# Performance work log

Hardware: AMD Instinct MI355X
Metric: run time of the kernel (lower is better)

Reference implementation:

```python
import jax, jax.numpy as jnp
import numpy as np

T = 3          # num_node_type
B = 8          # batch
N = 512        # max_doc_len
F_IN = 256     # in_features
F_OUT = 128    # out_features
NE = 10        # num_edge_type (embedding has NE+1 rows, row 0 = padding)
ALPHA = 0.2    # leaky relu slope
NEG = -9e15    # masked-score fill, same constant as torch source


def setup_inputs() -> dict:
    key = jax.random.key(0)
    ks = jax.random.split(key, 7)
    node_rep = jax.random.normal(ks[0], (B, N, F_IN), jnp.float32)
    node_type_mask_rep = jax.random.uniform(ks[1], (T, B, N, 1), jnp.float32)
    adj = jax.random.randint(ks[2], (B, N, N), 0, NE + 1, jnp.int32)
    W = jax.random.normal(ks[3], (T, F_IN, F_OUT), jnp.float32) * 0.05
    b = jnp.zeros((T, F_OUT), jnp.float32)
    # attention vector a in R^{2F} split into halves (GAT trick): a([h_i, x2_ij]) = h_i.a1 + x2_ij.a2 + a_b
    a1 = jax.random.normal(ks[4], (F_OUT,), jnp.float32) * 0.05
    a2 = jax.random.normal(ks[5], (F_OUT,), jnp.float32) * 0.05
    a_b = jnp.zeros((), jnp.float32)
    emb = jax.random.normal(ks[6], (NE + 1, F_OUT), jnp.float32) * 0.05
    emb = emb.at[0].set(0.0)  # padding_idx=0
    return {"node_rep": node_rep, "node_type_mask_rep": node_type_mask_rep,
            "adj": adj, "W": W, "b": b, "a1": a1, "a2": a2, "a_b": a_b, "emb": emb}


def reference(node_rep, node_type_mask_rep, adj, W, b, a1, a2, a_b, emb):
    # typed projection: h = sum_t (node_rep @ W_t + b_t) * mask_t   -> (B, N, F_OUT)
    h = jnp.sum((jnp.einsum('bni,tio->tbno', node_rep, W) + b[:, None, None, :])
                * node_type_mask_rep, axis=0)
    # edge-type embeddings: (B, N, N, F_OUT)
    E = emb[adj]
    # x_2[b,i,j] = h[b,j] + E[b,i,j]
    x2 = h[:, None, :, :] + E
    # score[b,i,j] = leakyrelu(a1.h_i + a2.x2_ij + a_b)  (decomposed concat-linear)
    s = (jnp.einsum('bif,f->bi', h, a1)[:, :, None]
         + jnp.einsum('bijf,f->bij', x2, a2) + a_b)
    s = jnp.where(s > 0, s, ALPHA * s)
    s = jnp.where(adj > 0, s, jnp.float32(NEG))
    attn = jax.nn.softmax(s, axis=2)
    # weighted sum over neighbors of x_2 (NOT h), then ELU
    out = jnp.einsum('bij,bijf->bif', attn, x2)
    return jax.nn.elu(out)
```

## Files before the change

kernel.cpp:

```cpp
#include <hip/hip_runtime.h>

constexpr int kB    = 8;
constexpr int kN    = 512;
constexpr int kFIN  = 256;
constexpr int kFOUT = 128;
constexpr int kNE   = 10;
constexpr int kBN   = kB * kN;
constexpr float kALPHA = 0.2f;
constexpr float kNEG   = -9e15f;

typedef __attribute__((ext_vector_type(8))) short bhalf8;
typedef __attribute__((ext_vector_type(4))) float f32x4;

__device__ __forceinline__ unsigned short bf16_trunc(float x) {
    union { float f; unsigned u; } c; c.f = x;
    return (unsigned short)(c.u >> 16);
}
__device__ __forceinline__ float bf16_tof(unsigned short h) {
    union { unsigned u; float f; } c; c.u = ((unsigned)h) << 16;
    return c.f;
}

__global__ __launch_bounds__(256) void prep_kernel(
    const float* __restrict__ node_rep,
    const float* __restrict__ W,
    unsigned short* __restrict__ Xh,
    unsigned short* __restrict__ Xl,
    unsigned short* __restrict__ Whp,
    unsigned short* __restrict__ Wlp)
{
    const int tid = threadIdx.x;
    if (blockIdx.x < 1024) {
        const int gid  = blockIdx.x * 256 + tid;
        const size_t base = (size_t)gid * 4;
        const float4 v = *(const float4*)&node_rep[base];
        ushort4 hi, lo;
        float t;
        hi.x = bf16_trunc(v.x); t = v.x - bf16_tof(hi.x); lo.x = bf16_trunc(t);
        hi.y = bf16_trunc(v.y); t = v.y - bf16_tof(hi.y); lo.y = bf16_trunc(t);
        hi.z = bf16_trunc(v.z); t = v.z - bf16_tof(hi.z); lo.z = bf16_trunc(t);
        hi.w = bf16_trunc(v.w); t = v.w - bf16_tof(hi.w); lo.w = bf16_trunc(t);
        *(ushort4*)&Xh[base] = hi;
        *(ushort4*)&Xl[base] = lo;
    } else {
        const int g    = (blockIdx.x - 1024) * 256 + tid;
        const int lane = g & 63;
        const int nt   = (g >> 6) & 7;
        const int ks   = (g >> 9) & 7;
        const int tt   = g >> 12;
        const int col  = nt * 16 + (lane & 15);
        const int kb   = ks * 32 + ((lane >> 4) * 8);
        unsigned short hbuf[8], lbuf[8];
        #pragma unroll
        for (int j = 0; j < 8; ++j) {
            const float w = W[((size_t)tt * kFIN + kb + j) * kFOUT + col];
            hbuf[j] = bf16_trunc(w);
            lbuf[j] = bf16_trunc(w - bf16_tof(hbuf[j]));
        }
        const size_t dst = ((size_t)((tt * 8 + ks) * 8 + nt)) * 512 + lane * 8;
        #pragma unroll
        for (int j = 0; j < 8; ++j) { Whp[dst + j] = hbuf[j]; Wlp[dst + j] = lbuf[j]; }
    }
}

__global__ __launch_bounds__(256) void proj_mfma_kernel(
    const unsigned short* __restrict__ Xh,
    const unsigned short* __restrict__ Xl,
    const unsigned short* __restrict__ Whp,
    const unsigned short* __restrict__ Wlp,
    float* __restrict__ y)
{
    const int tid   = threadIdx.x;
    const int t     = blockIdx.x % 3;
    const int rb    = blockIdx.x / 3;
    const int wave  = tid >> 6;
    const int lane  = tid & 63;
    const int wrow  = wave & 1;
    const int whalf = wave >> 1;

    const int rowA = rb * 32 + wrow * 16 + (lane & 15);
    const unsigned short* xhp = Xh + (size_t)rowA * kFIN + ((lane >> 4) * 8);
    const unsigned short* xlp = Xl + (size_t)rowA * kFIN + ((lane >> 4) * 8);

    f32x4 acc[4] = {{0,0,0,0},{0,0,0,0},{0,0,0,0},{0,0,0,0}};

    #pragma unroll
    for (int ks = 0; ks < 8; ++ks) {
        const bhalf8 Ah = *(const bhalf8*)(xhp + ks * 32);
        const bhalf8 Al = *(const bhalf8*)(xlp + ks * 32);
        const size_t bw = ((size_t)((t * 8 + ks) * 8 + whalf * 4)) * 512 + lane * 8;
        #pragma unroll
        for (int n = 0; n < 4; ++n) {
            const bhalf8 Bh = *(const bhalf8*)(Whp + bw + n * 512);
            const bhalf8 Bl = *(const bhalf8*)(Wlp + bw + n * 512);
            acc[n] = __builtin_amdgcn_mfma_f32_16x16x32_bf16(Ah, Bh, acc[n], 0, 0, 0);
            acc[n] = __builtin_amdgcn_mfma_f32_16x16x32_bf16(Ah, Bl, acc[n], 0, 0, 0);
            acc[n] = __builtin_amdgcn_mfma_f32_16x16x32_bf16(Al, Bh, acc[n], 0, 0, 0);
        }
    }

    const int rbase = rb * 32 + wrow * 16 + ((lane >> 4) * 4);
    const int cbase = whalf * 64 + (lane & 15);
    #pragma unroll
    for (int n = 0; n < 4; ++n)
        #pragma unroll
        for (int j = 0; j < 4; ++j)
            y[((size_t)t * kBN + rbase + j) * kFOUT + cbase + n * 16] = acc[n][j];
}

__global__ __launch_bounds__(256) void reduce_kernel(
    const float* __restrict__ y,
    const float* __restrict__ mask,
    const float* __restrict__ bias,
    const float* __restrict__ a1,
    const float* __restrict__ a2,
    const float* __restrict__ a_b,
    const float* __restrict__ emb,
    float* __restrict__ h,
    float* __restrict__ s1,
    float* __restrict__ s2,
    float* __restrict__ emb_a2)
{
    __shared__ float hls[8][kFOUT];

    const int tid  = threadIdx.x;
    const int row0 = blockIdx.x * 8;
    const int o    = tid & 127;
    const int rh   = tid >> 7;

    #pragma unroll
    for (int rr = 0; rr < 4; ++rr) {
        const int r   = rh * 4 + rr;
        const int row = row0 + r;
        const float hv =
              mask[0 * kBN + row] * (y[((size_t)0 * kBN + row) * kFOUT + o] + bias[0 * kFOUT + o])
            + mask[1 * kBN + row] * (y[((size_t)1 * kBN + row) * kFOUT + o] + bias[1 * kFOUT + o])
            + mask[2 * kBN + row] * (y[((size_t)2 * kBN + row) * kFOUT + o] + bias[2 * kFOUT + o]);
        h[(size_t)row * kFOUT + o] = hv;
        hls[r][o] = hv;
    }
    __syncthreads();

    {
        const int wv = tid >> 6, lane = tid & 63;
        #pragma unroll
        for (int rr = 0; rr < 2; ++rr) {
            const int r = wv * 2 + rr;
            const float v0 = hls[r][lane];
            const float v1 = hls[r][64 + lane];
            float p1 = v0 * a1[lane] + v1 * a1[64 + lane];
            float p2 = v0 * a2[lane] + v1 * a2[64 + lane];
            #pragma unroll
            for (int off = 32; off; off >>= 1) {
                p1 += __shfl_down(p1, off);
                p2 += __shfl_down(p2, off);
            }
            if (lane == 0) {
                s1[row0 + r] = p1 + a_b[0];
                s2[row0 + r] = p2;
            }
        }
    }

    if (blockIdx.x == 0 && tid < 176) {
        const int e = tid >> 4, l = tid & 15;
        float p = 0.f;
        #pragma unroll
        for (int k8 = 0; k8 < 8; ++k8)
            p += emb[e * kFOUT + l + k8 * 16] * a2[l + k8 * 16];
        #pragma unroll
        for (int off = 8; off; off >>= 1) p += __shfl_xor(p, off);
        if (l == 0) emb_a2[e] = p;
    }
}

__global__ __launch_bounds__(512) void attn_kernel(
    const int*   __restrict__ adj,
    const float* __restrict__ emb,
    const float* __restrict__ h,
    const float* __restrict__ s1,
    const float* __restrict__ s2,
    const float* __restrict__ emb_a2g,
    float* __restrict__ out)
{
    __shared__ float sc[8][kN + 4];
    __shared__ int   adjs[8][kN];
    __shared__ float scT[kN][8];
    __shared__ float wsum[8][16];
    __shared__ float ea2[16];

    const int tid = threadIdx.x;
    const int b   = blockIdx.x >> 6;
    const int i0  = (blockIdx.x & 63) * 8;

    if (tid < 16) ea2[tid] = emb_a2g[tid];
    __syncthreads();

    const int*   adjb = adj + ((size_t)(b * kN + i0)) * kN;
    const float* s2b  = s2 + b * kN;
    #pragma unroll
    for (int it = 0; it < 2; ++it) {
        const int idx = tid + it * 512;
        const int r = idx >> 7, jq = idx & 127;
        const int4   av  = *(const int4*)&adjb[(size_t)r * kN + jq * 4];
        const float4 s2v = *(const float4*)&s2b[jq * 4];
        const float  sr  = s1[b * kN + i0 + r];
        float4 sv; float s;
        s = sr + s2v.x + ea2[av.x]; s = s > 0.f ? s : kALPHA * s; sv.x = av.x > 0 ? s : kNEG;
        s = sr + s2v.y + ea2[av.y]; s = s > 0.f ? s : kALPHA * s; sv.y = av.y > 0 ? s : kNEG;
        s = sr + s2v.z + ea2[av.z]; s = s > 0.f ? s : kALPHA * s; sv.z = av.z > 0 ? s : kNEG;
        s = sr + s2v.w + ea2[av.w]; s = s > 0.f ? s : kALPHA * s; sv.w = av.w > 0 ? s : kNEG;
        *(float4*)&sc[r][jq * 4] = sv;
        *(int4*)&adjs[r][jq * 4] = av;
    }
    __syncthreads();

    {
        const int r = tid >> 6, lane = tid & 63;
        float v[8]; int av[8];
        #pragma unroll
        for (int k = 0; k < 8; ++k) {
            v[k]  = sc[r][lane + k * 64];
            av[k] = adjs[r][lane + k * 64];
        }
        float m = v[0];
        #pragma unroll
        for (int k = 1; k < 8; ++k) m = fmaxf(m, v[k]);
        #pragma unroll
        for (int off = 32; off; off >>= 1) m = fmaxf(m, __shfl_xor(m, off));
        float sum = 0.f;
        #pragma unroll
        for (int k = 0; k < 8; ++k) { v[k] = __expf(v[k] - m); sum += v[k]; }
        #pragma unroll
        for (int off = 32; off; off >>= 1) sum += __shfl_xor(sum, off);
        const float inv = 1.0f / sum;
        #pragma unroll
        for (int k = 0; k < 8; ++k) {
            v[k] *= inv;
            scT[lane + k * 64][r] = v[k];
        }
        #pragma unroll
        for (int e = 1; e <= kNE; ++e) {
            float p = 0.f;
            #pragma unroll
            for (int k = 0; k < 8; ++k) p += (av[k] == e) ? v[k] : 0.f;
            #pragma unroll
            for (int off = 32; off; off >>= 1) p += __shfl_xor(p, off);
            if (lane == 0) wsum[r][e] = p;
        }
    }
    __syncthreads();

    const int f4l = tid & 31;
    const int rg  = (tid >> 5) & 1;
    const int js  = tid >> 6;
    const float* hb  = h + ((size_t)(b * kN + js * 64)) * kFOUT + f4l * 4;
    const float* sct = &scT[js * 64][rg * 4];

    float4 acc0 = {0,0,0,0}, acc1 = {0,0,0,0}, acc2 = {0,0,0,0}, acc3 = {0,0,0,0};
    #pragma unroll 4
    for (int jj = 0; jj < 64; ++jj) {
        const float4 w4 = *(const float4*)&sct[jj * 8];
        const float4 hv = *(const float4*)&hb[(size_t)jj * kFOUT];
        acc0.x = fmaf(w4.x, hv.x, acc0.x); acc0.y = fmaf(w4.x, hv.y, acc0.y);
        acc0.z = fmaf(w4.x, hv.z, acc0.z); acc0.w = fmaf(w4.x, hv.w, acc0.w);
        acc1.x = fmaf(w4.y, hv.x, acc1.x); acc1.y = fmaf(w4.y, hv.y, acc1.y);
        acc1.z = fmaf(w4.y, hv.z, acc1.z); acc1.w = fmaf(w4.y, hv.w, acc1.w);
        acc2.x = fmaf(w4.z, hv.x, acc2.x); acc2.y = fmaf(w4.z, hv.y, acc2.y);
        acc2.z = fmaf(w4.z, hv.z, acc2.z); acc2.w = fmaf(w4.z, hv.w, acc2.w);
        acc3.x = fmaf(w4.w, hv.x, acc3.x); acc3.y = fmaf(w4.w, hv.y, acc3.y);
        acc3.z = fmaf(w4.w, hv.z, acc3.z); acc3.w = fmaf(w4.w, hv.w, acc3.w);
    }
    __syncthreads();

    float* parts_lo = (float*)adjs;
    float* parts_hi = (float*)sc;
    {
        float* pbase = (js < 4) ? parts_lo + js * 1024
                                : parts_hi + (js - 4) * 1024;
        const int rbase = rg * 4;
        *(float4*)&pbase[(rbase + 0) * kFOUT + f4l * 4] = acc0;
        *(float4*)&pbase[(rbase + 1) * kFOUT + f4l * 4] = acc1;
        *(float4*)&pbase[(rbase + 2) * kFOUT + f4l * 4] = acc2;
        *(float4*)&pbase[(rbase + 3) * kFOUT + f4l * 4] = acc3;
    }
    __syncthreads();

    if (tid < 256) {
        const int r  = tid >> 5;
        const int fl = (tid & 31) * 4;
        float4 a = {0,0,0,0};
        #pragma unroll
        for (int p = 0; p < 4; ++p) {
            const float4 v0 = *(const float4*)&parts_lo[p * 1024 + r * kFOUT + fl];
            const float4 v1 = *(const float4*)&parts_hi[p * 1024 + r * kFOUT + fl];
            a.x += v0.x + v1.x; a.y += v0.y + v1.y;
            a.z += v0.z + v1.z; a.w += v0.w + v1.w;
        }
        #pragma unroll
        for (int e = 1; e <= kNE; ++e) {
            const float  wv = wsum[r][e];
            const float4 ev = *(const float4*)&emb[e * kFOUT + fl];
            a.x = fmaf(wv, ev.x, a.x); a.y = fmaf(wv, ev.y, a.y);
            a.z = fmaf(wv, ev.z, a.z); a.w = fmaf(wv, ev.w, a.w);
        }
        a.x = a.x > 0.f ? a.x : expm1f(a.x);
        a.y = a.y > 0.f ? a.y : expm1f(a.y);
        a.z = a.z > 0.f ? a.z : expm1f(a.z);
        a.w = a.w > 0.f ? a.w : expm1f(a.w);
        *(float4*)&out[((size_t)(b * kN + i0 + r)) * kFOUT + fl] = a;
    }
}

extern "C" void kernel_launch(void* const* d_in, const int* in_sizes, int n_in,
                              void* d_out, int out_size, void* d_ws, size_t ws_size,
                              hipStream_t stream) {
    const float* node_rep = (const float*)d_in[0];
    const float* mask     = (const float*)d_in[1];
    const int*   adj      = (const int*)  d_in[2];
    const float* W        = (const float*)d_in[3];
    const float* bias     = (const float*)d_in[4];
    const float* a1       = (const float*)d_in[5];
    const float* a2       = (const float*)d_in[6];
    const float* a_b      = (const float*)d_in[7];
    const float* emb      = (const float*)d_in[8];
    float* out = (float*)d_out;

    float* fws    = (float*)d_ws;
    float* h      = fws;
    float* s1     = h + (size_t)kBN * kFOUT;
    float* s2     = s1 + kBN;
    float* emb_a2 = s2 + kBN;
    float* y      = emb_a2 + 64;
    unsigned short* Xh  = (unsigned short*)(y + (size_t)3 * kBN * kFOUT);
    unsigned short* Xl  = Xh + (size_t)kBN * kFIN;
    unsigned short* Whp = Xl + (size_t)kBN * kFIN;
    unsigned short* Wlp = Whp + 3 * 8 * 8 * 512;

    prep_kernel<<<1072, 256, 0, stream>>>(node_rep, W, Xh, Xl, Whp, Wlp);
    proj_mfma_kernel<<<384, 256, 0, stream>>>(Xh, Xl, Whp, Wlp, y);
    reduce_kernel<<<kBN / 8, 256, 0, stream>>>(
        y, mask, bias, a1, a2, a_b, emb, h, s1, s2, emb_a2);
    attn_kernel<<<kBN / 8, 512, 0, stream>>>(
        adj, emb, h, s1, s2, emb_a2, out);
}
```

Before: 108.7 us.

## Fuse bf16 split, typed projection and score reduction into one kernel

```diff
diff --git a/kernel.cpp b/kernel.cpp
--- a/kernel.cpp
+++ b/kernel.cpp
@@ -22,28 +22,16 @@
 }
 
 __global__ __launch_bounds__(256) void prep_kernel(
-    const float* __restrict__ node_rep,
     const float* __restrict__ W,
-    unsigned short* __restrict__ Xh,
-    unsigned short* __restrict__ Xl,
+    const float* __restrict__ emb,
+    const float* __restrict__ a2,
     unsigned short* __restrict__ Whp,
-    unsigned short* __restrict__ Wlp)
+    unsigned short* __restrict__ Wlp,
+    float* __restrict__ emb_a2)
 {
     const int tid = threadIdx.x;
-    if (blockIdx.x < 1024) {
-        const int gid  = blockIdx.x * 256 + tid;
-        const size_t base = (size_t)gid * 4;
-        const float4 v = *(const float4*)&node_rep[base];
-        ushort4 hi, lo;
-        float t;
-        hi.x = bf16_trunc(v.x); t = v.x - bf16_tof(hi.x); lo.x = bf16_trunc(t);
-        hi.y = bf16_trunc(v.y); t = v.y - bf16_tof(hi.y); lo.y = bf16_trunc(t);
-        hi.z = bf16_trunc(v.z); t = v.z - bf16_tof(hi.z); lo.z = bf16_trunc(t);
-        hi.w = bf16_trunc(v.w); t = v.w - bf16_tof(hi.w); lo.w = bf16_trunc(t);
-        *(ushort4*)&Xh[base] = hi;
-        *(ushort4*)&Xl[base] = lo;
-    } else {
-        const int g    = (blockIdx.x - 1024) * 256 + tid;
+    if (blockIdx.x < 48) {
+        const int g    = blockIdx.x * 256 + tid;
         const int lane = g & 63;
         const int nt   = (g >> 6) & 7;
         const int ks   = (g >> 9) & 7;
@@ -60,117 +48,120 @@
         const size_t dst = ((size_t)((tt * 8 + ks) * 8 + nt)) * 512 + lane * 8;
         #pragma unroll
         for (int j = 0; j < 8; ++j) { Whp[dst + j] = hbuf[j]; Wlp[dst + j] = lbuf[j]; }
-    }
-}
-
-__global__ __launch_bounds__(256) void proj_mfma_kernel(
-    const unsigned short* __restrict__ Xh,
-    const unsigned short* __restrict__ Xl,
+    } else if (tid < 176) {
+        const int e = tid >> 4, l = tid & 15;
+        float p = 0.f;
+        #pragma unroll
+        for (int k8 = 0; k8 < 8; ++k8)
+            p += emb[e * kFOUT + l + k8 * 16] * a2[l + k8 * 16];
+        #pragma unroll
+        for (int off = 8; off; off >>= 1) p += __shfl_xor(p, off);
+        if (l == 0) emb_a2[e] = p;
+    }
+}
+
+__global__ __launch_bounds__(512) void proj_kernel(
+    const float* __restrict__ node_rep,
+    const float* __restrict__ mask,
+    const float* __restrict__ bias,
     const unsigned short* __restrict__ Whp,
     const unsigned short* __restrict__ Wlp,
-    float* __restrict__ y)
-{
-    const int tid   = threadIdx.x;
-    const int t     = blockIdx.x % 3;
-    const int rb    = blockIdx.x / 3;
-    const int wave  = tid >> 6;
-    const int lane  = tid & 63;
-    const int wrow  = wave & 1;
-    const int whalf = wave >> 1;
-
-    const int rowA = rb * 32 + wrow * 16 + (lane & 15);
-    const unsigned short* xhp = Xh + (size_t)rowA * kFIN + ((lane >> 4) * 8);
-    const unsigned short* xlp = Xl + (size_t)rowA * kFIN + ((lane >> 4) * 8);
-
-    f32x4 acc[4] = {{0,0,0,0},{0,0,0,0},{0,0,0,0},{0,0,0,0}};
-
-    #pragma unroll
-    for (int ks = 0; ks < 8; ++ks) {
-        const bhalf8 Ah = *(const bhalf8*)(xhp + ks * 32);
-        const bhalf8 Al = *(const bhalf8*)(xlp + ks * 32);
-        const size_t bw = ((size_t)((t * 8 + ks) * 8 + whalf * 4)) * 512 + lane * 8;
-        #pragma unroll
-        for (int n = 0; n < 4; ++n) {
-            const bhalf8 Bh = *(const bhalf8*)(Whp + bw + n * 512);
-            const bhalf8 Bl = *(const bhalf8*)(Wlp + bw + n * 512);
-            acc[n] = __builtin_amdgcn_mfma_f32_16x16x32_bf16(Ah, Bh, acc[n], 0, 0, 0);
-            acc[n] = __builtin_amdgcn_mfma_f32_16x16x32_bf16(Ah, Bl, acc[n], 0, 0, 0);
-            acc[n] = __builtin_amdgcn_mfma_f32_16x16x32_bf16(Al, Bh, acc[n], 0, 0, 0);
-        }
-    }
-
-    const int rbase = rb * 32 + wrow * 16 + ((lane >> 4) * 4);
-    const int cbase = whalf * 64 + (lane & 15);
-    #pragma unroll
-    for (int n = 0; n < 4; ++n)
-        #pragma unroll
-        for (int j = 0; j < 4; ++j)
-            y[((size_t)t * kBN + rbase + j) * kFOUT + cbase + n * 16] = acc[n][j];
-}
-
-__global__ __launch_bounds__(256) void reduce_kernel(
-    const float* __restrict__ y,
-    const float* __restrict__ mask,
-    const float* __restrict__ bias,
     const float* __restrict__ a1,
     const float* __restrict__ a2,
     const float* __restrict__ a_b,
-    const float* __restrict__ emb,
     float* __restrict__ h,
     float* __restrict__ s1,
-    float* __restrict__ s2,
-    float* __restrict__ emb_a2)
+    float* __restrict__ s2)
 {
-    __shared__ float hls[8][kFOUT];
+    __shared__ short xsh[32][264];
+    __shared__ short xsl[32][264];
 
     const int tid  = threadIdx.x;
-    const int row0 = blockIdx.x * 8;
-    const int o    = tid & 127;
-    const int rh   = tid >> 7;
+    const int row0 = blockIdx.x * 32;
+
+    #pragma unroll
+    for (int it = 0; it < 4; ++it) {
+        const int idx = tid + it * 512;
+        const int r = idx >> 6, q = idx & 63;
+        const float4 v = *(const float4*)&node_rep[(size_t)(row0 + r) * kFIN + q * 4];
+        ushort4 hi, lo;
+        hi.x = bf16_trunc(v.x); lo.x = bf16_trunc(v.x - bf16_tof(hi.x));
+        hi.y = bf16_trunc(v.y); lo.y = bf16_trunc(v.y - bf16_tof(hi.y));
+        hi.z = bf16_trunc(v.z); lo.z = bf16_trunc(v.z - bf16_tof(hi.z));
+        hi.w = bf16_trunc(v.w); lo.w = bf16_trunc(v.w - bf16_tof(hi.w));
+        *(ushort4*)&xsh[r][q * 4] = hi;
+        *(ushort4*)&xsl[r][q * 4] = lo;
+    }
+    __syncthreads();
+
+    const int wave = tid >> 6, lane = tid & 63;
+    const int wrow = wave & 1, wcol = wave >> 1;
+    const int arow = wrow * 16 + (lane & 15);
+    const int koff = (lane >> 4) * 8;
+
+    f32x4 acc[3][2];
+    #pragma unroll
+    for (int t = 0; t < 3; ++t)
+        #pragma unroll
+        for (int nt = 0; nt < 2; ++nt) acc[t][nt] = (f32x4){0,0,0,0};
+
+    #pragma unroll 2
+    for (int ks = 0; ks < 8; ++ks) {
+        const bhalf8 Ah = *(const bhalf8*)&xsh[arow][ks * 32 + koff];
+        const bhalf8 Al = *(const bhalf8*)&xsl[arow][ks * 32 + koff];
+        #pragma unroll
+        for (int t = 0; t < 3; ++t)
+            #pragma unroll
+            for (int nt = 0; nt < 2; ++nt) {
+                const size_t bw =
+                    ((size_t)((t * 8 + ks) * 8 + wcol * 2 + nt)) * 512 + lane * 8;
+                const bhalf8 Bh = *(const bhalf8*)(Whp + bw);
+                const bhalf8 Bl = *(const bhalf8*)(Wlp + bw);
+                acc[t][nt] = __builtin_amdgcn_mfma_f32_16x16x32_bf16(Ah, Bh, acc[t][nt], 0, 0, 0);
+                acc[t][nt] = __builtin_amdgcn_mfma_f32_16x16x32_bf16(Ah, Bl, acc[t][nt], 0, 0, 0);
+                acc[t][nt] = __builtin_amdgcn_mfma_f32_16x16x32_bf16(Al, Bh, acc[t][nt], 0, 0, 0);
+            }
+    }
+    __syncthreads();
+
+    float* hstash = (float*)xsh;
+
+    const int rA = wrow * 16 + ((lane >> 4) * 4);
+    const int cA = lane & 15;
+    #pragma unroll
+    for (int j = 0; j < 4; ++j) {
+        const int row = row0 + rA + j;
+        const float m0 = mask[row];
+        const float m1 = mask[kBN + row];
+        const float m2 = mask[2 * kBN + row];
+        #pragma unroll
+        for (int nt = 0; nt < 2; ++nt) {
+            const int col = wcol * 32 + nt * 16 + cA;
+            const float hv = m0 * (acc[0][nt][j] + bias[col])
+                           + m1 * (acc[1][nt][j] + bias[kFOUT + col])
+                           + m2 * (acc[2][nt][j] + bias[2 * kFOUT + col]);
+            h[(size_t)row * kFOUT + col] = hv;
+            hstash[(rA + j) * 132 + col] = hv;
+        }
+    }
+    __syncthreads();
 
     #pragma unroll
     for (int rr = 0; rr < 4; ++rr) {
-        const int r   = rh * 4 + rr;
-        const int row = row0 + r;
-        const float hv =
-              mask[0 * kBN + row] * (y[((size_t)0 * kBN + row) * kFOUT + o] + bias[0 * kFOUT + o])
-            + mask[1 * kBN + row] * (y[((size_t)1 * kBN + row) * kFOUT + o] + bias[1 * kFOUT + o])
-            + mask[2 * kBN + row] * (y[((size_t)2 * kBN + row) * kFOUT + o] + bias[2 * kFOUT + o]);
-        h[(size_t)row * kFOUT + o] = hv;
-        hls[r][o] = hv;
-    }
-    __syncthreads();
-
-    {
-        const int wv = tid >> 6, lane = tid & 63;
-        #pragma unroll
-        for (int rr = 0; rr < 2; ++rr) {
-            const int r = wv * 2 + rr;
-            const float v0 = hls[r][lane];
-            const float v1 = hls[r][64 + lane];
-            float p1 = v0 * a1[lane] + v1 * a1[64 + lane];
-            float p2 = v0 * a2[lane] + v1 * a2[64 + lane];
-            #pragma unroll
-            for (int off = 32; off; off >>= 1) {
-                p1 += __shfl_down(p1, off);
-                p2 += __shfl_down(p2, off);
-            }
-            if (lane == 0) {
-                s1[row0 + r] = p1 + a_b[0];
-                s2[row0 + r] = p2;
-            }
-        }
-    }
-
-    if (blockIdx.x == 0 && tid < 176) {
-        const int e = tid >> 4, l = tid & 15;
-        float p = 0.f;
-        #pragma unroll
-        for (int k8 = 0; k8 < 8; ++k8)
-            p += emb[e * kFOUT + l + k8 * 16] * a2[l + k8 * 16];
-        #pragma unroll
-        for (int off = 8; off; off >>= 1) p += __shfl_xor(p, off);
-        if (l == 0) emb_a2[e] = p;
+        const int r = wave * 4 + rr;
+        const float v0 = hstash[r * 132 + lane];
+        const float v1 = hstash[r * 132 + 64 + lane];
+        float p1 = v0 * a1[lane] + v1 * a1[64 + lane];
+        float p2 = v0 * a2[lane] + v1 * a2[64 + lane];
+        #pragma unroll
+        for (int off = 32; off; off >>= 1) {
+            p1 += __shfl_down(p1, off);
+            p2 += __shfl_down(p2, off);
+        }
+        if (lane == 0) {
+            s1[row0 + r] = p1 + a_b[0];
+            s2[row0 + r] = p2;
+        }
     }
 }
 
@@ -331,16 +322,12 @@
     float* s1     = h + (size_t)kBN * kFOUT;
     float* s2     = s1 + kBN;
     float* emb_a2 = s2 + kBN;
-    float* y      = emb_a2 + 64;
-    unsigned short* Xh  = (unsigned short*)(y + (size_t)3 * kBN * kFOUT);
-    unsigned short* Xl  = Xh + (size_t)kBN * kFIN;
-    unsigned short* Whp = Xl + (size_t)kBN * kFIN;
+    unsigned short* Whp = (unsigned short*)(emb_a2 + 64);
     unsigned short* Wlp = Whp + 3 * 8 * 8 * 512;
 
-    prep_kernel<<<1072, 256, 0, stream>>>(node_rep, W, Xh, Xl, Whp, Wlp);
-    proj_mfma_kernel<<<384, 256, 0, stream>>>(Xh, Xl, Whp, Wlp, y);
-    reduce_kernel<<<kBN / 8, 256, 0, stream>>>(
-        y, mask, bias, a1, a2, a_b, emb, h, s1, s2, emb_a2);
+    prep_kernel<<<49, 256, 0, stream>>>(W, emb, a2, Whp, Wlp, emb_a2);
+    proj_kernel<<<kBN / 32, 512, 0, stream>>>(
+        node_rep, mask, bias, Whp, Wlp, a1, a2, a_b, h, s1, s2);
     attn_kernel<<<kBN / 8, 512, 0, stream>>>(
         adj, emb, h, s1, s2, emb_a2, out);
 }
```

Measured after the change: 111.5 us. 2.6% more time.
